# Kernel optimization log

Measured on AMD Instinct MI355X. Metric: run time of the kernel, lower is better.

## Reference

```python
import jax, jax.numpy as jnp
import numpy as np

B, N, M = 64, 256, 16
ONF, OEF = 92, 41
NF, EF = 128, 64
FINAL = 128  # final_node_len; final_layer outputs FINAL//2


def _linear_params(key, fan_in, fan_out):
    # kaiming_uniform fan_in, relu: bound = sqrt(6/fan_in)
    bound = np.sqrt(6.0 / fan_in)
    W = jax.random.uniform(key, (fan_out, fan_in), jnp.float32, -bound, bound)
    b = jnp.zeros((fan_out,), jnp.float32)
    return W, b


def setup_inputs() -> dict:
    key = jax.random.key(0)
    ks = jax.random.split(key, 12)
    node_fea = jax.random.normal(ks[0], (B, N, ONF), jnp.float32)
    edge_fea = jax.random.normal(ks[1], (B, N, M, OEF), jnp.float32)
    edge_fea_idx = jax.random.randint(ks[2], (B, N, M), 0, N)
    dis = jax.random.uniform(ks[3], (N, N), jnp.float32)
    Wn, bn = _linear_params(ks[4], ONF, NF)
    We, be = _linear_params(ks[5], OEF, EF)
    W1, b1 = _linear_params(ks[6], 2 * NF + EF, 2 * NF)
    W2, b2 = _linear_params(ks[7], 2 * NF + EF, 2 * NF)
    W3, b3 = _linear_params(ks[8], 2 * NF + EF, 2 * NF)
    Wf, bf = _linear_params(ks[9], NF, FINAL // 2)
    return dict(node_fea=node_fea, edge_fea=edge_fea, edge_fea_idx=edge_fea_idx,
                dis=dis, Wn=Wn, bn=bn, We=We, be=be,
                W1=W1, b1=b1, a1=jnp.float32(0.7),
                W2=W2, b2=b2, a2=jnp.float32(0.7),
                W3=W3, b3=b3, a3=jnp.float32(0.7),
                Wf=Wf, bf=bf,
                DAw=jnp.float32(48.0 / 5.0), DAb=jnp.float32(-28.0 / 5.0))


def _conv(nf, ef, idx, W, b, alpha):
    # nf: [B,N,F]; ef: [B,N,M,E]; idx: [B,N,M]
    Bb, Nn, Mm = idx.shape
    F = nf.shape[-1]
    idx_c = jnp.maximum(idx, 0)
    gathered = jax.vmap(lambda x, i: x[i])(nf, idx_c)           # [B,N,M,F]
    self_exp = jnp.broadcast_to(nf[:, :, None, :], (Bb, Nn, Mm, F))
    total = jnp.concatenate([self_exp, gathered, ef], axis=-1)   # [B,N,M,2F+E]
    gated = jnp.einsum('bnmi,oi->bnmo', total, W) + b            # [B,N,M,2F]
    nbr_filter, nbr_core = jnp.split(gated, 2, axis=-1)
    mask = (idx >= 0).astype(nf.dtype)[..., None]
    nbr_filter = jax.nn.sigmoid(nbr_filter) * mask
    nbr_core = jax.nn.softplus(nbr_core)
    nbr_sumed = jnp.sum(nbr_filter * nbr_core, axis=2)           # [B,N,F]
    return jax.nn.softplus(alpha * nf + nbr_sumed)


def reference(node_fea, edge_fea, edge_fea_idx, dis,
              Wn, bn, We, be,
              W1, b1, a1, W2, b2, a2, W3, b3, a3,
              Wf, bf, DAw, DAb):
    nf = node_fea @ Wn.T + bn                                    # [B,N,NF]
    ef = edge_fea @ We.T + be                                    # [B,N,M,EF]
    nf = _conv(nf, ef, edge_fea_idx, W1, b1, a1)
    nf = _conv(nf, ef, edge_fea_idx, W2, b2, a2)
    nf = _conv(nf, ef, edge_fea_idx, W3, b3, a3)
    nf = nf @ Wf.T + bf                                          # [B,N,FINAL//2]
    DA = jax.nn.sigmoid(DAw * dis + DAb)                         # [N,N]
    node1 = jnp.einsum('ij,bjf->bif', DA, nf)
    return jnp.concatenate([nf, node1], axis=2)                  # [B,N,FINAL]
```

## Files before the change

### kernel.cpp

```cpp
#include <hip/hip_runtime.h>
#include <hip/hip_bf16.h>
#include <math.h>

#define Bb   64
#define Nn   256
#define Mm   16
#define ONF  92
#define OEF  41
#define NF   128
#define EF   64
#define KDIM 320
#define ODIM 256
#define FINAL 128
#define K0C  6

typedef __attribute__((ext_vector_type(8))) short short8;
typedef __attribute__((ext_vector_type(4))) float f32x4;

__device__ __forceinline__ float sigmoidf_(float x) {
    float e = __expf(-x);
    return __builtin_amdgcn_rcpf(1.0f + e);
}
__device__ __forceinline__ float softplusf_(float x) {
    return fmaxf(x, 0.0f) + __logf(1.0f + __expf(-fabsf(x)));
}
__device__ __forceinline__ __hip_bfloat16 to_bf16(float x) { return __float2bfloat16(x); }

__device__ __forceinline__ void swz(const float* __restrict__ in, __hip_bfloat16* __restrict__ out,
                                    int t, int Itot, int koff, int Kuse, int K0)
{
    int j = t & 7;
    int u = t >> 3;
    int lane = u & 63;
    int ln16 = lane & 15, q = lane >> 4;
    int v = u >> 6;
    int k0 = v % K0, tile = v / K0;
    int n = tile * 16 + ln16, k = k0 * 32 + q * 8 + j;
    out[t] = (k < Kuse) ? to_bf16(in[(size_t)n * Itot + koff + k]) : to_bf16(0.0f);
}

#define SZ_WET (OEF * EF)
#define SZ_WB  (16 * K0C * 512)
#define SZ_WS  (16 * 4 * 512)
#define SZ_WNB ((NF / 16) * 3 * 512)
#define SZ_WEB ((EF / 16) * 2 * 512)
#define SZ_WFB ((64 / 16) * 4 * 512)
#define SZ_DA  (Nn * Nn)
#define PREP_TOTAL (SZ_WET + 3 * SZ_WB + 3 * SZ_WS + SZ_WNB + SZ_WEB + SZ_WFB + SZ_DA)

__global__ __launch_bounds__(256) void k_prep(
    const float* __restrict__ We, const float* __restrict__ W1,
    const float* __restrict__ W2, const float* __restrict__ W3,
    const float* __restrict__ Wn, const float* __restrict__ Wf,
    const float* __restrict__ dis, const float* __restrict__ pw, const float* __restrict__ pb,
    float* __restrict__ WeT,
    __hip_bfloat16* __restrict__ W1b, __hip_bfloat16* __restrict__ W2b, __hip_bfloat16* __restrict__ W3b,
    __hip_bfloat16* __restrict__ W1s, __hip_bfloat16* __restrict__ W2s, __hip_bfloat16* __restrict__ W3s,
    __hip_bfloat16* __restrict__ Wnb, __hip_bfloat16* __restrict__ Web, __hip_bfloat16* __restrict__ Wfb,
    __hip_bfloat16* __restrict__ DAf)
{
    int t = blockIdx.x * 256 + threadIdx.x;
    if (t < SZ_WET) {
        int o = t / OEF, i = t - o * OEF;
        WeT[i * EF + o] = We[t];
        return;
    }
    t -= SZ_WET;
    if (t < SZ_WB) { swz(W1, W1b, t, KDIM, NF, 192, K0C); return; }
    t -= SZ_WB;
    if (t < SZ_WB) { swz(W2, W2b, t, KDIM, NF, 192, K0C); return; }
    t -= SZ_WB;
    if (t < SZ_WB) { swz(W3, W3b, t, KDIM, NF, 192, K0C); return; }
    t -= SZ_WB;
    if (t < SZ_WS) { swz(W1, W1s, t, KDIM, 0, NF, 4); return; }
    t -= SZ_WS;
    if (t < SZ_WS) { swz(W2, W2s, t, KDIM, 0, NF, 4); return; }
    t -= SZ_WS;
    if (t < SZ_WS) { swz(W3, W3s, t, KDIM, 0, NF, 4); return; }
    t -= SZ_WS;
    if (t < SZ_WNB) { swz(Wn, Wnb, t, ONF, 0, ONF, 3); return; }
    t -= SZ_WNB;
    if (t < SZ_WEB) { swz(We, Web, t, OEF, 0, OEF, 2); return; }
    t -= SZ_WEB;
    if (t < SZ_WFB) { swz(Wf, Wfb, t, NF, 0, NF, 4); return; }
    t -= SZ_WFB;
    if (t < SZ_DA) {
        int i = t >> 8, jx = t & 255;
        float v = sigmoidf_(fmaf(*pw, dis[t], *pb));
        int itile = i >> 4, ln16 = i & 15;
        int k0 = jx >> 5, q = (jx >> 3) & 3, jj = jx & 7;
        DAf[(size_t)((((itile * 8 + k0) << 6) + (q << 4) + ln16)) * 8 + jj] = to_bf16(v);
    }
}

template<int KIN, int K0, int NCOLS>
__device__ __forceinline__ void emb_body(
    int bid, const float* __restrict__ X, const __hip_bfloat16* __restrict__ Bswz,
    const float* __restrict__ bias, __hip_bfloat16* __restrict__ Y,
    __hip_bfloat16* A_s, __hip_bfloat16* O_s)
{
    constexpr int KP = K0 * 32;
    constexpr int TPW = NCOLS / 64;
    constexpr int OLD = NCOLS + 24;

    const int row0 = bid * 64;
    const int t = threadIdx.x;

    {
        const float4* Xb = (const float4*)(X + (size_t)row0 * KIN);
        constexpr int NV = (64 * KIN) / 4;
        for (int c = t; c < NV; c += 256) {
            float4 v = Xb[c];
            int flat = c * 4;
            #pragma unroll
            for (int e = 0; e < 4; e++) {
                int f = flat + e;
                int row = f / KIN, k = f - row * KIN;
                int mt = row >> 4, ln16 = row & 15;
                int k0 = k >> 5, q = (k >> 3) & 3, j = k & 7;
                float vv = (e == 0) ? v.x : (e == 1) ? v.y : (e == 2) ? v.z : v.w;
                A_s[(((mt * K0 + k0) << 6) + (q << 4) + ln16) * 8 + j] = to_bf16(vv);
            }
        }
        constexpr int PAD = KP - KIN;
        for (int c = t; c < 64 * PAD; c += 256) {
            int row = c / PAD, k = KIN + (c - row * PAD);
            int mt = row >> 4, ln16 = row & 15;
            int k0 = k >> 5, q = (k >> 3) & 3, j = k & 7;
            A_s[(((mt * K0 + k0) << 6) + (q << 4) + ln16) * 8 + j] = to_bf16(0.0f);
        }
    }
    __syncthreads();

    const int wv = t >> 6, lane = t & 63;
    const int q = lane >> 4, ln16 = lane & 15;

    f32x4 acc[4][TPW];
    #pragma unroll
    for (int p = 0; p < TPW; p++) {
        float bv = bias[(wv * TPW + p) * 16 + ln16];
        #pragma unroll
        for (int mt = 0; mt < 4; mt++) acc[mt][p] = (f32x4){bv, bv, bv, bv};
    }

    short8 bw[TPW][K0];
    #pragma unroll
    for (int p = 0; p < TPW; p++)
        #pragma unroll
        for (int k0 = 0; k0 < K0; k0++)
            bw[p][k0] = *(const short8*)(Bswz + ((size_t)((wv * TPW + p) * K0 + k0) << 9) + (lane << 3));

    #pragma unroll
    for (int k0 = 0; k0 < K0; k0++) {
        short8 af[4];
        #pragma unroll
        for (int mt = 0; mt < 4; mt++)
            af[mt] = *(const short8*)(A_s + (((mt * K0 + k0) << 6) + lane) * 8);
        #pragma unroll
        for (int mt = 0; mt < 4; mt++)
            #pragma unroll
            for (int p = 0; p < TPW; p++)
                acc[mt][p] = __builtin_amdgcn_mfma_f32_16x16x32_bf16(af[mt], bw[p][k0], acc[mt][p], 0, 0, 0);
    }

    #pragma unroll
    for (int mt = 0; mt < 4; mt++)
        #pragma unroll
        for (int p = 0; p < TPW; p++) {
            int col = (wv * TPW + p) * 16 + ln16;
            #pragma unroll
            for (int r = 0; r < 4; r++)
                O_s[(mt * 16 + q * 4 + r) * OLD + col] = to_bf16(acc[mt][p][r]);
        }
    __syncthreads();
    constexpr int CH = NCOLS / 8;
    for (int c = t; c < 64 * CH; c += 256) {
        int row = c / CH, ch = c - row * CH;
        *(uint4*)(Y + (size_t)(row0 + row) * NCOLS + ch * 8) =
            *(const uint4*)(O_s + row * OLD + ch * 8);
    }
}

__global__ __launch_bounds__(256) void k_embed_all(
    const float* __restrict__ node_fea, const __hip_bfloat16* __restrict__ Wnb,
    const float* __restrict__ bn, __hip_bfloat16* __restrict__ nf0,
    const float* __restrict__ edge_fea, const __hip_bfloat16* __restrict__ Web,
    const float* __restrict__ be, __hip_bfloat16* __restrict__ efb)
{
    __shared__ __align__(16) __hip_bfloat16 A_s[4 * 3 * 512];
    __shared__ __align__(16) __hip_bfloat16 O_s[64 * (NF + 24)];
    if (blockIdx.x < 256)
        emb_body<ONF, 3, NF>(blockIdx.x, node_fea, Wnb, bn, nf0, A_s, O_s);
    else
        emb_body<OEF, 2, EF>(blockIdx.x - 256, edge_fea, Web, be, efb, A_s, O_s);
}

template<bool PRECOMP>
__global__ __launch_bounds__(256, 3) void k_conv_mfma(
    const __hip_bfloat16* __restrict__ nf_in,
    const float* __restrict__ edge_fea,
    const __hip_bfloat16* __restrict__ ef_bf,
    const int*   __restrict__ eidx,
    const float* __restrict__ WeT,
    const float* __restrict__ be,
    const __hip_bfloat16* __restrict__ Wb,
    const __hip_bfloat16* __restrict__ Wsb,
    const float* __restrict__ bias,
    const float* __restrict__ palpha,
    __hip_bfloat16* __restrict__ nf_out)
{
    __shared__ __align__(16) __hip_bfloat16 A_s[4 * K0C * 512];
    __shared__ __align__(16) __hip_bfloat16 A_sf[4 * 512];

    const int node0 = blockIdx.x * 4;
    const int b = node0 >> 8;
    const int t = threadIdx.x;
    const int wv = t >> 6, lane = t & 63;
    const int q = lane >> 4, ln16 = lane & 15;
    const int row = (wv << 4) + ln16;

    const int myidx = eidx[node0 * Mm + row];
    const unsigned long long mball = __ballot(eidx[node0 * Mm + lane] >= 0);

    {
        int j = myidx < 0 ? 0 : myidx;
        const __hip_bfloat16* gathp = nf_in + (size_t)((b << 8) + j) * NF;
        #pragma unroll
        for (int k0 = 0; k0 < 4; k0++)
            *(uint4*)(A_s + ((wv * K0C + k0) * 64 + lane) * 8) =
                *(const uint4*)(gathp + k0 * 32 + q * 8);
        if (lane < 16)
            *(uint4*)(A_sf + (((lane >> 2) * 64) + (lane & 3) * 16 + wv) * 8) =
                *(const uint4*)(nf_in + (size_t)(node0 + wv) * NF + lane * 8);
        if (PRECOMP) {
            const __hip_bfloat16* efp = ef_bf + (size_t)((node0 << 4) + row) * EF;
            #pragma unroll
            for (int k0 = 0; k0 < 2; k0++)
                *(uint4*)(A_s + ((wv * K0C + 4 + k0) * 64 + lane) * 8) =
                    *(const uint4*)(efp + k0 * 32 + q * 8);
        } else {
            for (int c = t; c < 64 * EF; c += 256) {
                int rr = c >> 6, col = c & 63;
                float a = be[col];
                const float* er = edge_fea + (size_t)(node0 * Mm + rr) * OEF;
                #pragma unroll
                for (int i = 0; i < OEF; i++) a = fmaf(er[i], WeT[i * EF + col], a);
                int mt = rr >> 4, l16 = rr & 15;
                int k0 = 4 + (col >> 5), qq = (col >> 3) & 3, jj = col & 7;
                A_s[((mt * K0C + k0) * 64 + qq * 16 + l16) * 8 + jj] = to_bf16(a);
            }
        }
    }
    __syncthreads();

    f32x4 sv[4];
    #pragma unroll
    for (int c = 0; c < 4; c++) {
        int tile = 2 * wv + (c & 1) + ((c >> 1) << 3);
        float bv = bias[tile * 16 + ln16];
        sv[c] = (f32x4){bv, bv, bv, bv};
    }
    #pragma unroll
    for (int k0 = 0; k0 < 4; k0++) {
        short8 afs = *(const short8*)(A_sf + (k0 * 64 + lane) * 8);
        #pragma unroll
        for (int c = 0; c < 4; c++) {
            int tile = 2 * wv + (c & 1) + ((c >> 1) << 3);
            short8 bws = *(const short8*)(Wsb + ((size_t)(tile * 4 + k0) << 9) + (lane << 3));
            sv[c] = __builtin_amdgcn_mfma_f32_16x16x32_bf16(afs, bws, sv[c], 0, 0, 0);
        }
    }

    f32x4 accF[4][2], accC[4][2];
    #pragma unroll
    for (int mt = 0; mt < 4; mt++) {
        #pragma unroll
        for (int p = 0; p < 2; p++) {
            float vF = __shfl(sv[p][mt], ln16);
            float vC = __shfl(sv[2 + p][mt], ln16);
            accF[mt][p] = (f32x4){vF, vF, vF, vF};
            accC[mt][p] = (f32x4){vC, vC, vC, vC};
        }
    }

    const __hip_bfloat16* WF0 = Wb + ((size_t)(2 * wv) * (K0C * 512)) + (lane << 3);
    const __hip_bfloat16* WF1 = WF0 + K0C * 512;
    const __hip_bfloat16* WC0 = WF0 + 8 * (K0C * 512);
    const __hip_bfloat16* WC1 = WC0 + K0C * 512;

    #pragma unroll
    for (int k0 = 0; k0 < K0C; k0++) {
        short8 cF0 = *(const short8*)(WF0 + k0 * 512);
        short8 cF1 = *(const short8*)(WF1 + k0 * 512);
        short8 cC0 = *(const short8*)(WC0 + k0 * 512);
        short8 cC1 = *(const short8*)(WC1 + k0 * 512);
        short8 af[4];
        #pragma unroll
        for (int mt = 0; mt < 4; mt++)
            af[mt] = *(const short8*)(A_s + ((mt * K0C + k0) * 64 + lane) * 8);
        #pragma unroll
        for (int mt = 0; mt < 4; mt++) {
            accF[mt][0] = __builtin_amdgcn_mfma_f32_16x16x32_bf16(af[mt], cF0, accF[mt][0], 0, 0, 0);
            accF[mt][1] = __builtin_amdgcn_mfma_f32_16x16x32_bf16(af[mt], cF1, accF[mt][1], 0, 0, 0);
            accC[mt][0] = __builtin_amdgcn_mfma_f32_16x16x32_bf16(af[mt], cC0, accC[mt][0], 0, 0, 0);
            accC[mt][1] = __builtin_amdgcn_mfma_f32_16x16x32_bf16(af[mt], cC1, accC[mt][1], 0, 0, 0);
        }
    }

    const float alpha = *palpha;
    #pragma unroll
    for (int mt = 0; mt < 4; mt++) {
        const int gnode = node0 + mt;
        #pragma unroll
        for (int p = 0; p < 2; p++) {
            float partial = 0.0f;
            #pragma unroll
            for (int r = 0; r < 4; r++) {
                bool msk = (mball >> (mt * 16 + q * 4 + r)) & 1ull;
                float f = sigmoidf_(accF[mt][p][r]);
                float c = softplusf_(accC[mt][p][r]);
                partial += msk ? f * c : 0.0f;
            }
            partial += __shfl_xor(partial, 16);
            partial += __shfl_xor(partial, 32);
            if (q == 0) {
                int col = (2 * wv + p) * 16 + ln16;
                float self = __bfloat162float(nf_in[(size_t)gnode * NF + col]);
                nf_out[(size_t)gnode * NF + col] = to_bf16(softplusf_(fmaf(alpha, self, partial)));
            }
        }
    }
}

__global__ __launch_bounds__(256) void k_final_mfma(
    const __hip_bfloat16* __restrict__ nf, const __hip_bfloat16* __restrict__ Wfb,
    const float* __restrict__ bfv, float* __restrict__ out,
    __hip_bfloat16* __restrict__ XT)
{
    __shared__ __align__(16) __hip_bfloat16 A_s[16 * 512];
    const int node0 = blockIdx.x * 64;
    const int bloc = node0 >> 8;
    const int t = threadIdx.x;
    const int wv = t >> 6, lane = t & 63;
    const int q = lane >> 4, ln16 = lane & 15;

    const __hip_bfloat16* rowp = nf + (size_t)(node0 + (wv << 4) + ln16) * NF;
    #pragma unroll
    for (int k0 = 0; k0 < 4; k0++)
        *(uint4*)(A_s + ((wv * 4 + k0) * 64 + lane) * 8) =
            *(const uint4*)(rowp + k0 * 32 + q * 8);
    __syncthreads();

    short8 bw[4];
    #pragma unroll
    for (int k0 = 0; k0 < 4; k0++)
        bw[k0] = *(const short8*)(Wfb + ((size_t)(wv * 4 + k0) * 64 + lane) * 8);

    float bv = bfv[wv * 16 + ln16];
    f32x4 acc[4];
    #pragma unroll
    for (int mt = 0; mt < 4; mt++) acc[mt] = (f32x4){bv, bv, bv, bv};

    #pragma unroll
    for (int k0 = 0; k0 < 4; k0++) {
        short8 af[4];
        #pragma unroll
        for (int mt = 0; mt < 4; mt++)
            af[mt] = *(const short8*)(A_s + ((mt * 4 + k0) * 64 + lane) * 8);
        #pragma unroll
        for (int mt = 0; mt < 4; mt++)
            acc[mt] = __builtin_amdgcn_mfma_f32_16x16x32_bf16(af[mt], bw[k0], acc[mt], 0, 0, 0);
    }

    const int col = (wv << 4) + ln16;
    #pragma unroll
    for (int mt = 0; mt < 4; mt++)
        #pragma unroll
        for (int r = 0; r < 4; r++) {
            int row = mt * 16 + q * 4 + r;
            float v = acc[mt][r];
            out[(size_t)(node0 + row) * FINAL + col] = v;
            XT[(size_t)(bloc * 64 + col) * 256 + (node0 & 255) + row] = to_bf16(v);
        }
}

__global__ __launch_bounds__(256) void k_node1_mfma(
    const __hip_bfloat16* __restrict__ DAf,
    const __hip_bfloat16* __restrict__ XT,
    float* __restrict__ out)
{
    __shared__ __align__(16) __hip_bfloat16 B_s[32 * 512];
    const int blk = blockIdx.x;
    const int b = blk >> 2, i0 = (blk & 3) * 64;
    const int t = threadIdx.x;
    const int wv = t >> 6, lane = t & 63;
    const int q = lane >> 4, ln16 = lane & 15;

    const __hip_bfloat16* xrow = XT + (size_t)(b * 64 + (wv << 4) + ln16) * 256;
    #pragma unroll
    for (int k0 = 0; k0 < 8; k0++)
        *(uint4*)(B_s + ((wv * 8 + k0) * 64 + lane) * 8) =
            *(const uint4*)(xrow + k0 * 32 + q * 8);
    __syncthreads();

    f32x4 acc[4];
    #pragma unroll
    for (int mt = 0; mt < 4; mt++) acc[mt] = (f32x4){0.f, 0.f, 0.f, 0.f};

    #pragma unroll
    for (int k0 = 0; k0 < 8; k0++) {
        short8 bfr = *(const short8*)(B_s + ((wv * 8 + k0) * 64 + lane) * 8);
        short8 af[4];
        #pragma unroll
        for (int mt = 0; mt < 4; mt++)
            af[mt] = *(const short8*)(DAf + (size_t)(((i0 >> 4) + mt) * 8 + k0) * 512 + (lane << 3));
        #pragma unroll
        for (int mt = 0; mt < 4; mt++)
            acc[mt] = __builtin_amdgcn_mfma_f32_16x16x32_bf16(af[mt], bfr, acc[mt], 0, 0, 0);
    }

    #pragma unroll
    for (int mt = 0; mt < 4; mt++)
        #pragma unroll
        for (int r = 0; r < 4; r++) {
            int i = i0 + mt * 16 + q * 4 + r;
            out[(size_t)((b << 8) + i) * FINAL + 64 + (wv << 4) + ln16] = acc[mt][r];
        }
}

extern "C" void kernel_launch(void* const* d_in, const int* in_sizes, int n_in,
                              void* d_out, int out_size, void* d_ws, size_t ws_size,
                              hipStream_t stream)
{
    const float* node_fea = (const float*)d_in[0];
    const float* edge_fea = (const float*)d_in[1];
    const int*   eidx     = (const int*)  d_in[2];
    const float* dis      = (const float*)d_in[3];
    const float* Wn = (const float*)d_in[4];
    const float* bn = (const float*)d_in[5];
    const float* We = (const float*)d_in[6];
    const float* be = (const float*)d_in[7];
    const float* W1 = (const float*)d_in[8];
    const float* b1 = (const float*)d_in[9];
    const float* a1 = (const float*)d_in[10];
    const float* W2 = (const float*)d_in[11];
    const float* b2 = (const float*)d_in[12];
    const float* a2 = (const float*)d_in[13];
    const float* W3 = (const float*)d_in[14];
    const float* b3 = (const float*)d_in[15];
    const float* a3 = (const float*)d_in[16];
    const float* Wf = (const float*)d_in[17];
    const float* bf = (const float*)d_in[18];
    const float* DAw = (const float*)d_in[19];
    const float* DAb = (const float*)d_in[20];
    float* out = (float*)d_out;

    char* base = (char*)d_ws;
    size_t off = 0;
    auto alloc = [&](size_t bytes) { char* p = base + off; off = (off + bytes + 255) & ~(size_t)255; return p; };
    __hip_bfloat16* nfA = (__hip_bfloat16*)alloc((size_t)Bb * Nn * NF * 2);
    __hip_bfloat16* nfB = (__hip_bfloat16*)alloc((size_t)Bb * Nn * NF * 2);
    __hip_bfloat16* W1b = (__hip_bfloat16*)alloc((size_t)SZ_WB * 2);
    __hip_bfloat16* W2b = (__hip_bfloat16*)alloc((size_t)SZ_WB * 2);
    __hip_bfloat16* W3b = (__hip_bfloat16*)alloc((size_t)SZ_WB * 2);
    __hip_bfloat16* W1s = (__hip_bfloat16*)alloc((size_t)SZ_WS * 2);
    __hip_bfloat16* W2s = (__hip_bfloat16*)alloc((size_t)SZ_WS * 2);
    __hip_bfloat16* W3s = (__hip_bfloat16*)alloc((size_t)SZ_WS * 2);
    float* WeT = (float*)alloc((size_t)OEF * EF * 4);
    __hip_bfloat16* DAf = (__hip_bfloat16*)alloc((size_t)Nn * Nn * 2);
    __hip_bfloat16* Wnb = (__hip_bfloat16*)alloc((size_t)SZ_WNB * 2);
    __hip_bfloat16* Web = (__hip_bfloat16*)alloc((size_t)SZ_WEB * 2);
    __hip_bfloat16* Wfb = (__hip_bfloat16*)alloc((size_t)SZ_WFB * 2);
    __hip_bfloat16* XT  = (__hip_bfloat16*)alloc((size_t)Bb * 64 * Nn * 2);
    __hip_bfloat16* efb = (__hip_bfloat16*)alloc((size_t)Bb * Nn * Mm * EF * 2);
    const bool precomp = (ws_size >= off);

    hipLaunchKernelGGL(k_prep, dim3((PREP_TOTAL + 255) / 256), dim3(256), 0, stream,
                       We, W1, W2, W3, Wn, Wf, dis, DAw, DAb,
                       WeT, W1b, W2b, W3b, W1s, W2s, W3s, Wnb, Web, Wfb, DAf);

    hipLaunchKernelGGL(k_embed_all, dim3(precomp ? (256 + Bb * Nn * Mm / 64) : 256), dim3(256), 0, stream,
                       node_fea, Wnb, bn, nfA, edge_fea, Web, be, efb);

    if (precomp) {
        hipLaunchKernelGGL((k_conv_mfma<true>), dim3(Bb * Nn / 4), dim3(256), 0, stream,
                           nfA, edge_fea, efb, eidx, WeT, be, W1b, W1s, b1, a1, nfB);
        hipLaunchKernelGGL((k_conv_mfma<true>), dim3(Bb * Nn / 4), dim3(256), 0, stream,
                           nfB, edge_fea, efb, eidx, WeT, be, W2b, W2s, b2, a2, nfA);
        hipLaunchKernelGGL((k_conv_mfma<true>), dim3(Bb * Nn / 4), dim3(256), 0, stream,
                           nfA, edge_fea, efb, eidx, WeT, be, W3b, W3s, b3, a3, nfB);
    } else {
        hipLaunchKernelGGL((k_conv_mfma<false>), dim3(Bb * Nn / 4), dim3(256), 0, stream,
                           nfA, edge_fea, efb, eidx, WeT, be, W1b, W1s, b1, a1, nfB);
        hipLaunchKernelGGL((k_conv_mfma<false>), dim3(Bb * Nn / 4), dim3(256), 0, stream,
                           nfB, edge_fea, efb, eidx, WeT, be, W2b, W2s, b2, a2, nfA);
        hipLaunchKernelGGL((k_conv_mfma<false>), dim3(Bb * Nn / 4), dim3(256), 0, stream,
                           nfA, edge_fea, efb, eidx, WeT, be, W3b, W3s, b3, a3, nfB);
    }

    hipLaunchKernelGGL(k_final_mfma, dim3(Bb * Nn / 64), dim3(256), 0, stream, nfB, Wfb, bf, out, XT);
    hipLaunchKernelGGL(k_node1_mfma, dim3(Bb * 4), dim3(256), 0, stream, DAf, XT, out);
}
```

Before: 308.8 us.

## Double conv block to eight waves, one output tile pair per wave

Each conv block now runs 512 threads (8 waves) instead of 256. Every wave computes one filter/core column-tile pair instead of two, and holds all of its weight fragments in registers before the MFMA loop. The shared-memory fill is split so waves 0-3 gather neighbor rows while waves 4-7 load edge features and self features. The aim is more waves per CU to hide memory and MFMA latency, with lower per-wave register pressure. The cost is more blocks-per-CU contention for LDS and registers under the new launch bounds, plus duplicated per-block setup work.

```diff
diff --git a/kernel.cpp b/kernel.cpp
--- a/kernel.cpp
+++ b/kernel.cpp
@@ -196,7 +196,7 @@
 }
 
 template<bool PRECOMP>
-__global__ __launch_bounds__(256, 3) void k_conv_mfma(
+__global__ __launch_bounds__(512, 4) void k_conv_mfma(
     const __hip_bfloat16* __restrict__ nf_in,
     const float* __restrict__ edge_fea,
     const __hip_bfloat16* __restrict__ ef_bf,
@@ -217,93 +217,98 @@
     const int t = threadIdx.x;
     const int wv = t >> 6, lane = t & 63;
     const int q = lane >> 4, ln16 = lane & 15;
-    const int row = (wv << 4) + ln16;
-
-    const int myidx = eidx[node0 * Mm + row];
+
     const unsigned long long mball = __ballot(eidx[node0 * Mm + lane] >= 0);
 
+    if (wv < 4) {
+        const int v = wv;
+        int j = eidx[(node0 + v) * Mm + ln16];
+        j = j < 0 ? 0 : j;
+        const __hip_bfloat16* gathp = nf_in + (size_t)((b << 8) + j) * NF;
+        #pragma unroll
+        for (int k0 = 0; k0 < 4; k0++)
+            *(uint4*)(A_s + ((v * K0C + k0) * 64 + lane) * 8) =
+                *(const uint4*)(gathp + k0 * 32 + q * 8);
+    } else {
+        const int v = wv - 4;
+        if (PRECOMP) {
+            if (lane < 32) {
+                const int q2 = q;
+                const __hip_bfloat16* efp = ef_bf + (size_t)((node0 << 4) + v * 16 + ln16) * EF;
+                #pragma unroll
+                for (int qq = 0; qq < 4; qq++)
+                    *(uint4*)(A_s + ((v * K0C + 4 + q2) * 64 + qq * 16 + ln16) * 8) =
+                        *(const uint4*)(efp + q2 * 32 + qq * 8);
+            } else if (lane < 48) {
+                const int c = ln16;
+                *(uint4*)(A_sf + (((c >> 2) * 64) + (c & 3) * 16 + v) * 8) =
+                    *(const uint4*)(nf_in + (size_t)(node0 + v) * NF + c * 8);
+            }
+        } else {
+            if (lane >= 32 && lane < 48) {
+                const int c = ln16;
+                *(uint4*)(A_sf + (((c >> 2) * 64) + (c & 3) * 16 + v) * 8) =
+                    *(const uint4*)(nf_in + (size_t)(node0 + v) * NF + c * 8);
+            }
+        }
+    }
+    if (!PRECOMP) {
+        for (int c = t; c < 64 * EF; c += 512) {
+            int rr = c >> 6, col = c & 63;
+            float a = be[col];
+            const float* er = edge_fea + (size_t)(node0 * Mm + rr) * OEF;
+            #pragma unroll
+            for (int i = 0; i < OEF; i++) a = fmaf(er[i], WeT[i * EF + col], a);
+            int mt = rr >> 4, l16 = rr & 15;
+            int k0 = 4 + (col >> 5), qq = (col >> 3) & 3, jj = col & 7;
+            A_s[((mt * K0C + k0) * 64 + qq * 16 + l16) * 8 + jj] = to_bf16(a);
+        }
+    }
+    __syncthreads();
+
+    f32x4 sv0, sv1;
     {
-        int j = myidx < 0 ? 0 : myidx;
-        const __hip_bfloat16* gathp = nf_in + (size_t)((b << 8) + j) * NF;
-        #pragma unroll
-        for (int k0 = 0; k0 < 4; k0++)
-            *(uint4*)(A_s + ((wv * K0C + k0) * 64 + lane) * 8) =
-                *(const uint4*)(gathp + k0 * 32 + q * 8);
-        if (lane < 16)
-            *(uint4*)(A_sf + (((lane >> 2) * 64) + (lane & 3) * 16 + wv) * 8) =
-                *(const uint4*)(nf_in + (size_t)(node0 + wv) * NF + lane * 8);
-        if (PRECOMP) {
-            const __hip_bfloat16* efp = ef_bf + (size_t)((node0 << 4) + row) * EF;
-            #pragma unroll
-            for (int k0 = 0; k0 < 2; k0++)
-                *(uint4*)(A_s + ((wv * K0C + 4 + k0) * 64 + lane) * 8) =
-                    *(const uint4*)(efp + k0 * 32 + q * 8);
-        } else {
-            for (int c = t; c < 64 * EF; c += 256) {
-                int rr = c >> 6, col = c & 63;
-                float a = be[col];
-                const float* er = edge_fea + (size_t)(node0 * Mm + rr) * OEF;
-                #pragma unroll
-                for (int i = 0; i < OEF; i++) a = fmaf(er[i], WeT[i * EF + col], a);
-                int mt = rr >> 4, l16 = rr & 15;
-                int k0 = 4 + (col >> 5), qq = (col >> 3) & 3, jj = col & 7;
-                A_s[((mt * K0C + k0) * 64 + qq * 16 + l16) * 8 + jj] = to_bf16(a);
-            }
-        }
-    }
-    __syncthreads();
-
-    f32x4 sv[4];
-    #pragma unroll
-    for (int c = 0; c < 4; c++) {
-        int tile = 2 * wv + (c & 1) + ((c >> 1) << 3);
-        float bv = bias[tile * 16 + ln16];
-        sv[c] = (f32x4){bv, bv, bv, bv};
+        float bF = bias[wv * 16 + ln16], bC = bias[(wv + 8) * 16 + ln16];
+        sv0 = (f32x4){bF, bF, bF, bF};
+        sv1 = (f32x4){bC, bC, bC, bC};
     }
     #pragma unroll
     for (int k0 = 0; k0 < 4; k0++) {
         short8 afs = *(const short8*)(A_sf + (k0 * 64 + lane) * 8);
-        #pragma unroll
-        for (int c = 0; c < 4; c++) {
-            int tile = 2 * wv + (c & 1) + ((c >> 1) << 3);
-            short8 bws = *(const short8*)(Wsb + ((size_t)(tile * 4 + k0) << 9) + (lane << 3));
-            sv[c] = __builtin_amdgcn_mfma_f32_16x16x32_bf16(afs, bws, sv[c], 0, 0, 0);
-        }
-    }
-
-    f32x4 accF[4][2], accC[4][2];
+        short8 bws0 = *(const short8*)(Wsb + ((size_t)(wv * 4 + k0) << 9) + (lane << 3));
+        short8 bws1 = *(const short8*)(Wsb + ((size_t)((wv + 8) * 4 + k0) << 9) + (lane << 3));
+        sv0 = __builtin_amdgcn_mfma_f32_16x16x32_bf16(afs, bws0, sv0, 0, 0, 0);
+        sv1 = __builtin_amdgcn_mfma_f32_16x16x32_bf16(afs, bws1, sv1, 0, 0, 0);
+    }
+
+    f32x4 accF[4], accC[4];
     #pragma unroll
     for (int mt = 0; mt < 4; mt++) {
-        #pragma unroll
-        for (int p = 0; p < 2; p++) {
-            float vF = __shfl(sv[p][mt], ln16);
-            float vC = __shfl(sv[2 + p][mt], ln16);
-            accF[mt][p] = (f32x4){vF, vF, vF, vF};
-            accC[mt][p] = (f32x4){vC, vC, vC, vC};
-        }
-    }
-
-    const __hip_bfloat16* WF0 = Wb + ((size_t)(2 * wv) * (K0C * 512)) + (lane << 3);
-    const __hip_bfloat16* WF1 = WF0 + K0C * 512;
-    const __hip_bfloat16* WC0 = WF0 + 8 * (K0C * 512);
-    const __hip_bfloat16* WC1 = WC0 + K0C * 512;
-
+        float vF = __shfl(sv0[mt], ln16);
+        float vC = __shfl(sv1[mt], ln16);
+        accF[mt] = (f32x4){vF, vF, vF, vF};
+        accC[mt] = (f32x4){vC, vC, vC, vC};
+    }
+
+    const __hip_bfloat16* WF = Wb + ((size_t)wv * (K0C * 512)) + (lane << 3);
+    const __hip_bfloat16* WC = Wb + ((size_t)(wv + 8) * (K0C * 512)) + (lane << 3);
+    short8 bwF[K0C], bwC[K0C];
     #pragma unroll
     for (int k0 = 0; k0 < K0C; k0++) {
-        short8 cF0 = *(const short8*)(WF0 + k0 * 512);
-        short8 cF1 = *(const short8*)(WF1 + k0 * 512);
-        short8 cC0 = *(const short8*)(WC0 + k0 * 512);
-        short8 cC1 = *(const short8*)(WC1 + k0 * 512);
+        bwF[k0] = *(const short8*)(WF + k0 * 512);
+        bwC[k0] = *(const short8*)(WC + k0 * 512);
+    }
+
+    #pragma unroll
+    for (int k0 = 0; k0 < K0C; k0++) {
         short8 af[4];
         #pragma unroll
         for (int mt = 0; mt < 4; mt++)
             af[mt] = *(const short8*)(A_s + ((mt * K0C + k0) * 64 + lane) * 8);
         #pragma unroll
         for (int mt = 0; mt < 4; mt++) {
-            accF[mt][0] = __builtin_amdgcn_mfma_f32_16x16x32_bf16(af[mt], cF0, accF[mt][0], 0, 0, 0);
-            accF[mt][1] = __builtin_amdgcn_mfma_f32_16x16x32_bf16(af[mt], cF1, accF[mt][1], 0, 0, 0);
-            accC[mt][0] = __builtin_amdgcn_mfma_f32_16x16x32_bf16(af[mt], cC0, accC[mt][0], 0, 0, 0);
-            accC[mt][1] = __builtin_amdgcn_mfma_f32_16x16x32_bf16(af[mt], cC1, accC[mt][1], 0, 0, 0);
+            accF[mt] = __builtin_amdgcn_mfma_f32_16x16x32_bf16(af[mt], bwF[k0], accF[mt], 0, 0, 0);
+            accC[mt] = __builtin_amdgcn_mfma_f32_16x16x32_bf16(af[mt], bwC[k0], accC[mt], 0, 0, 0);
         }
     }
 
@@ -311,23 +316,20 @@
     #pragma unroll
     for (int mt = 0; mt < 4; mt++) {
         const int gnode = node0 + mt;
-        #pragma unroll
-        for (int p = 0; p < 2; p++) {
-            float partial = 0.0f;
-            #pragma unroll
-            for (int r = 0; r < 4; r++) {
-                bool msk = (mball >> (mt * 16 + q * 4 + r)) & 1ull;
-                float f = sigmoidf_(accF[mt][p][r]);
-                float c = softplusf_(accC[mt][p][r]);
-                partial += msk ? f * c : 0.0f;
-            }
-            partial += __shfl_xor(partial, 16);
-            partial += __shfl_xor(partial, 32);
-            if (q == 0) {
-                int col = (2 * wv + p) * 16 + ln16;
-                float self = __bfloat162float(nf_in[(size_t)gnode * NF + col]);
-                nf_out[(size_t)gnode * NF + col] = to_bf16(softplusf_(fmaf(alpha, self, partial)));
-            }
+        float partial = 0.0f;
+        #pragma unroll
+        for (int r = 0; r < 4; r++) {
+            bool msk = (mball >> (mt * 16 + q * 4 + r)) & 1ull;
+            float f = sigmoidf_(accF[mt][r]);
+            float c = softplusf_(accC[mt][r]);
+            partial += msk ? f * c : 0.0f;
+        }
+        partial += __shfl_xor(partial, 16);
+        partial += __shfl_xor(partial, 32);
+        if (q == 0) {
+            int col = wv * 16 + ln16;
+            float self = __bfloat162float(nf_in[(size_t)gnode * NF + col]);
+            nf_out[(size_t)gnode * NF + col] = to_bf16(softplusf_(fmaf(alpha, self, partial)));
         }
     }
 }
@@ -483,18 +485,18 @@
                        node_fea, Wnb, bn, nfA, edge_fea, Web, be, efb);
 
     if (precomp) {
-        hipLaunchKernelGGL((k_conv_mfma<true>), dim3(Bb * Nn / 4), dim3(256), 0, stream,
+        hipLaunchKernelGGL((k_conv_mfma<true>), dim3(Bb * Nn / 4), dim3(512), 0, stream,
                            nfA, edge_fea, efb, eidx, WeT, be, W1b, W1s, b1, a1, nfB);
-        hipLaunchKernelGGL((k_conv_mfma<true>), dim3(Bb * Nn / 4), dim3(256), 0, stream,
+        hipLaunchKernelGGL((k_conv_mfma<true>), dim3(Bb * Nn / 4), dim3(512), 0, stream,
                            nfB, edge_fea, efb, eidx, WeT, be, W2b, W2s, b2, a2, nfA);
-        hipLaunchKernelGGL((k_conv_mfma<true>), dim3(Bb * Nn / 4), dim3(256), 0, stream,
+        hipLaunchKernelGGL((k_conv_mfma<true>), dim3(Bb * Nn / 4), dim3(512), 0, stream,
                            nfA, edge_fea, efb, eidx, WeT, be, W3b, W3s, b3, a3, nfB);
     } else {
-        hipLaunchKernelGGL((k_conv_mfma<false>), dim3(Bb * Nn / 4), dim3(256), 0, stream,
+        hipLaunchKernelGGL((k_conv_mfma<false>), dim3(Bb * Nn / 4), dim3(512), 0, stream,
                            nfA, edge_fea, efb, eidx, WeT, be, W1b, W1s, b1, a1, nfB);
-        hipLaunchKernelGGL((k_conv_mfma<false>), dim3(Bb * Nn / 4), dim3(256), 0, stream,
+        hipLaunchKernelGGL((k_conv_mfma<false>), dim3(Bb * Nn / 4), dim3(512), 0, stream,
                            nfB, edge_fea, efb, eidx, WeT, be, W2b, W2s, b2, a2, nfA);
-        hipLaunchKernelGGL((k_conv_mfma<false>), dim3(Bb * Nn / 4), dim3(256), 0, stream,
+        hipLaunchKernelGGL((k_conv_mfma<false>), dim3(Bb * Nn / 4), dim3(512), 0, stream,
                            nfA, edge_fea, efb, eidx, WeT, be, W3b, W3s, b3, a3, nfB);
     }
 
```

After: 314.8 us. No clear change (+1.9%).
